# Kernel optimization log

Measured on AMD Instinct MI355X. Metric: run time of the kernel, lower is better.

## Reference

```python
import jax, jax.numpy as jnp
import numpy as np
import math

B, S, D = 8, 1024, 1024
NH, NKV, HD = 16, 8, 64
BLK_NUM, BLK_SIZE = 128, 8

def apply_rope(x, cos, sin):
    # x: (B,S,H,HD); cos/sin: (S, HD//2)
    x1 = x[..., 0::2]
    x2 = x[..., 1::2]
    c = cos[None, :, None, :]
    s = sin[None, :, None, :]
    r1 = x1 * c - x2 * s
    r2 = x1 * s + x2 * c
    out = jnp.stack([r1, r2], axis=-1).reshape(x.shape)
    return out

def setup_inputs() -> dict:
    key = jax.random.key(0)
    ks = jax.random.split(key, 7)
    x = jax.random.normal(ks[0], (B, S, D), dtype=jnp.float32)
    scale = 1.0 / math.sqrt(D)
    wq = jax.random.normal(ks[1], (D, NH * HD), dtype=jnp.float32) * scale
    wk = jax.random.normal(ks[2], (D, NKV * HD), dtype=jnp.float32) * scale
    wv = jax.random.normal(ks[3], (D, NKV * HD), dtype=jnp.float32) * scale
    wo = jax.random.normal(ks[4], (NH * HD, D), dtype=jnp.float32) * scale
    pos = jnp.arange(S, dtype=jnp.float32)
    inv_freq = 1.0 / (10000.0 ** (jnp.arange(0, HD, 2, dtype=jnp.float32) / HD))
    ang = pos[:, None] * inv_freq[None, :]
    freqs_cis_cos = jnp.cos(ang)
    freqs_cis_sin = jnp.sin(ang)
    return {"x": x, "wq": wq, "wk": wk, "wv": wv, "wo": wo,
            "freqs_cis_cos": freqs_cis_cos, "freqs_cis_sin": freqs_cis_sin,
            "start_pos": 0}

def reference(x, wq, wk, wv, wo, freqs_cis_cos, freqs_cis_sin, start_pos):
    q = (x @ wq).reshape(B, S, NH, HD)
    k = (x @ wk).reshape(B, S, NKV, HD)
    v = (x @ wv).reshape(B, S, NKV, HD)
    q = apply_rope(q, freqs_cis_cos, freqs_cis_sin)
    k = apply_rope(k, freqs_cis_cos, freqs_cis_sin)
    # GQA: repeat kv heads
    rep = NH // NKV
    k = jnp.repeat(k, rep, axis=2)  # (B,S,NH,HD)
    v = jnp.repeat(v, rep, axis=2)
    # block-causal mask: q in block i attends to kv blocks j <= i
    blk_id = jnp.arange(S) // BLK_SIZE
    mask = blk_id[:, None] >= blk_id[None, :]  # (S,S)
    scores = jnp.einsum('bqhd,bkhd->bhqk', q, k) / math.sqrt(HD)
    scores = jnp.where(mask[None, None], scores, -jnp.inf)
    attn = jax.nn.softmax(scores, axis=-1)
    out = jnp.einsum('bhqk,bkhd->bqhd', attn, v).reshape(B, S, NH * HD)
    return out @ wo
```

## Files before the change

kernel.cpp:

```cpp
#include <hip/hip_runtime.h>
#include <cstdint>
#include <math.h>

#define B_   8
#define S_   1024
#define D_   1024
#define NH_  16
#define NKV_ 8
#define HD_  64
#define M_   (B_*S_)

using bf16   = __bf16;
using bf16x4 = __attribute__((ext_vector_type(4))) __bf16;
using bf16x8 = __attribute__((ext_vector_type(8))) __bf16;
using f32x4  = __attribute__((ext_vector_type(4))) float;

__device__ __forceinline__ void gll16(const bf16* g, const bf16* l) {
    __builtin_amdgcn_global_load_lds(
        (const __attribute__((address_space(1))) unsigned int*)(uintptr_t)g,
        (__attribute__((address_space(3))) unsigned int*)(uintptr_t)l,
        16, 0, 0);
}

__device__ __forceinline__ void vm_wait0()  { asm volatile("s_waitcnt vmcnt(0)"  ::: "memory"); }
__device__ __forceinline__ void vm_wait5()  { asm volatile("s_waitcnt vmcnt(5)"  ::: "memory"); }
__device__ __forceinline__ void vm_wait6()  { asm volatile("s_waitcnt vmcnt(6)"  ::: "memory"); }
__device__ __forceinline__ void bar()       { __builtin_amdgcn_s_barrier(); asm volatile("" ::: "memory"); }

__global__ void k_prep1(const float* __restrict__ x,
                        const float* __restrict__ wq, const float* __restrict__ wk,
                        const float* __restrict__ wv, const float* __restrict__ wo,
                        bf16* __restrict__ xb, bf16* __restrict__ wqkvT, bf16* __restrict__ woT) {
    __shared__ float tile[64 * 65];
    int bid = blockIdx.x;
    int t = threadIdx.x;
    if (bid < 8192) {
        int i = bid * 256 + t;
        float4 v = ((const float4*)x)[i];
        bf16x4 o = { (bf16)v.x, (bf16)v.y, (bf16)v.z, (bf16)v.w };
        ((bf16x4*)xb)[i] = o;
        return;
    }
    int b2 = bid - 8192;
    int bx = b2 % 48, by = b2 / 48;
    const int R = 1024;
    const float* in; bf16* out; int C, xo;
    if (bx < 16)      { in = wq; out = wqkvT;               C = 1024; xo = bx; }
    else if (bx < 24) { in = wk; out = wqkvT + 1024 * 1024; C = 512;  xo = bx - 16; }
    else if (bx < 32) { in = wv; out = wqkvT + 1536 * 1024; C = 512;  xo = bx - 24; }
    else              { in = wo; out = woT;                 C = 1024; xo = bx - 32; }
    int r0 = by * 64, c0 = xo * 64;
    #pragma unroll
    for (int it = 0; it < 16; ++it) {
        int idx = it * 256 + t;
        int r = idx >> 6, c = idx & 63;
        tile[r * 65 + c] = in[(size_t)(r0 + r) * C + c0 + c];
    }
    __syncthreads();
    #pragma unroll
    for (int it = 0; it < 16; ++it) {
        int idx = it * 256 + t;
        int c = idx >> 6, r = idx & 63;
        out[(size_t)(c0 + c) * R + r0 + r] = (bf16)tile[r * 65 + c];
    }
}

template <typename OutT, int NI>
__global__ __launch_bounds__(512, 2) void k_gemm8p(const bf16* __restrict__ A,
                                                   const bf16* __restrict__ Bt,
                                                   OutT* __restrict__ C, int M, int N, int K) {
    constexpr int BN = NI * 64;
    __shared__ __align__(16) bf16 aL2[2 * 256 * 64];
    __shared__ __align__(16) bf16 bL2[2 * BN * 64];
    const int t    = threadIdx.x;
    const int lane = t & 63;
    const int w    = t >> 6;
    const int quad = lane >> 4;
    const int l16  = lane & 15;
    const int wr   = w >> 2;
    const int wc   = w & 3;

    int bid = blockIdx.y * gridDim.x + blockIdx.x;
    int cpx = (gridDim.x * gridDim.y) >> 3;
    int sw  = (bid & 7) * cpx + (bid >> 3);
    int bx  = sw % gridDim.x, by = sw / gridDim.x;
    const int m0 = by * 256;
    const int n0 = bx * BN;

    f32x4 acc[8][NI] = {};

    auto stageA2 = [&](int kb, int dbuf, int itX, int itY) {
        const int k0 = kb << 6;
        #pragma unroll
        for (int u = 0; u < 2; ++u) {
            int it = u ? itY : itX;
            int ci = it * 512 + t;
            int r = ci >> 3, c = ci & 7;
            int cg = c ^ (r & 7);
            gll16(A + (size_t)(m0 + r) * K + k0 + cg * 8, aL2 + dbuf * (256 * 64) + ci * 8);
        }
    };
    auto stageBh = [&](int kb, int dbuf, int nh) {
        const int k0 = kb << 6;
        #pragma unroll
        for (int j = 0; j < NI / 2; ++j) {
            int it = nh * (NI / 2) + j;
            int ci = it * 512 + t;
            int lr = ci >> 3, cs = ci & 7;
            int cg = cs ^ (lr & 7);
            int idx = lr - nh * (BN / 2);
            int wcc = idx / (NI * 8);
            int off = idx % (NI * 8);
            int g   = wcc * (NI * 16) + nh * (NI * 8) + off;
            gll16(Bt + (size_t)(n0 + g) * K + k0 + cg * 8, bL2 + dbuf * (BN * 64) + ci * 8);
        }
    };

    auto loadA = [&](const bf16* aL, int mh, bf16x8 (&af)[8]) {
        #pragma unroll
        for (int mi = 0; mi < 4; ++mi)
            #pragma unroll
            for (int kk = 0; kk < 2; ++kk) {
                int row = wr * 128 + (mh * 4 + mi) * 16 + l16;
                int ch  = (kk * 4 + quad) ^ (row & 7);
                af[mi * 2 + kk] = *(const bf16x8*)&aL[row * 64 + ch * 8];
            }
    };
    auto loadB = [&](const bf16* bL, int nh, bf16x8 (&bfr)[NI]) {
        #pragma unroll
        for (int j = 0; j < NI / 2; ++j)
            #pragma unroll
            for (int kk = 0; kk < 2; ++kk) {
                int lr = nh * (BN / 2) + wc * (NI * 8) + j * 16 + l16;
                int ch = (kk * 4 + quad) ^ (lr & 7);
                bfr[j * 2 + kk] = *(const bf16x8*)&bL[lr * 64 + ch * 8];
            }
    };
    auto mmac = [&](int mh, int nh, bf16x8 (&af)[8], bf16x8 (&bfr)[NI]) {
        __builtin_amdgcn_s_setprio(1);
        #pragma unroll
        for (int mi = 0; mi < 4; ++mi)
            #pragma unroll
            for (int j = 0; j < NI / 2; ++j)
                #pragma unroll
                for (int kk = 0; kk < 2; ++kk)
                    acc[mh * 4 + mi][nh * (NI / 2) + j] =
                        __builtin_amdgcn_mfma_f32_16x16x32_bf16(af[mi * 2 + kk], bfr[j * 2 + kk],
                                                                acc[mh * 4 + mi][nh * (NI / 2) + j], 0, 0, 0);
        __builtin_amdgcn_s_setprio(0);
    };

    const int NT = K >> 6;

    auto tile = [&](int T, int bufc) {
        const bf16* aL = aL2 + bufc * (256 * 64);
        const bf16* bL = bL2 + bufc * (BN * 64);
        bf16x8 af[8], bfr[NI];
        loadA(aL, 0, af); loadB(bL, 0, bfr);
        if (T + 1 < NT) stageBh(T + 1, bufc ^ 1, 1);
        bar();
        mmac(0, 0, af, bfr);
        bar();
        loadB(bL, 1, bfr);
        if (T + 2 < NT) stageA2(T + 2, bufc, 0, 2);
        bar();
        mmac(0, 1, af, bfr);
        bar();
        loadA(aL, 1, af); loadB(bL, 0, bfr);
        bar();
        mmac(1, 0, af, bfr);
        bar();
        loadB(bL, 1, bfr);
        if (T + 2 < NT) {
            stageA2(T + 2, bufc, 1, 3);
            stageBh(T + 2, bufc, 0);
            if constexpr (NI == 4) vm_wait6(); else vm_wait5();
        } else {
            vm_wait0();
        }
        bar();
        mmac(1, 1, af, bfr);
        bar();
    };

    stageA2(0, 0, 0, 2); stageA2(0, 0, 1, 3); stageBh(0, 0, 0); stageBh(0, 0, 1);
    stageA2(1, 1, 0, 2); stageA2(1, 1, 1, 3); stageBh(1, 1, 0);
    if constexpr (NI == 4) vm_wait6(); else vm_wait5();
    bar();

    for (int T = 0; T < NT; T += 2) {
        tile(T, 0);
        tile(T + 1, 1);
    }

    #pragma unroll
    for (int mi = 0; mi < 8; ++mi)
        #pragma unroll
        for (int ni = 0; ni < NI; ++ni)
            #pragma unroll
            for (int r = 0; r < 4; ++r) {
                int row = m0 + wr * 128 + mi * 16 + quad * 4 + r;
                int col = n0 + wc * (NI * 16) + ni * 16 + l16;
                C[(size_t)row * N + col] = (OutT)acc[mi][ni][r];
            }
}

__global__ void k_prep2(const bf16* __restrict__ qkv, const float* __restrict__ cosg,
                        const float* __restrict__ sing, bf16* __restrict__ qd,
                        bf16* __restrict__ kd, bf16* __restrict__ vt) {
    __shared__ __align__(16) bf16 tile[64 * 72];
    int bid = blockIdx.x;
    int t = threadIdx.x;
    if (bid < 8192) {
        if (t < 192) {
            int token = bid;
            int b = token >> 10, s = token & 1023;
            int hh = t >> 3, i8 = t & 7;
            float4 c4 = *(const float4*)&cosg[s * 32 + i8 * 4];
            float4 s4 = *(const float4*)&sing[s * 32 + i8 * 4];
            int srcBase, dstBase;
            bf16* dst;
            float sf;
            if (hh < 16) {
                srcBase = token * 2048 + hh * 64;
                dstBase = ((b * NH_ + hh) * S_ + s) * 64;
                dst = qd;
                sf = 0.180336879f;
            } else {
                int h = hh - 16;
                srcBase = token * 2048 + 1024 + h * 64;
                dstBase = ((b * NKV_ + h) * S_ + s) * 64;
                dst = kd;
                sf = 1.0f;
            }
            bf16x8 v = *(const bf16x8*)&qkv[srcBase + i8 * 8];
            const float cc[4] = { c4.x, c4.y, c4.z, c4.w };
            const float ss[4] = { s4.x, s4.y, s4.z, s4.w };
            bf16x8 o;
            #pragma unroll
            for (int j = 0; j < 4; ++j) {
                float e  = (float)v[2 * j];
                float od = (float)v[2 * j + 1];
                o[2 * j]     = (bf16)(sf * (e * cc[j] - od * ss[j]));
                o[2 * j + 1] = (bf16)(sf * (e * ss[j] + od * cc[j]));
            }
            *(bf16x8*)&dst[dstBase + i8 * 8] = o;
        }
        return;
    }
    int b2 = bid - 8192;
    int st = b2 & 15;
    int h  = (b2 >> 4) & 7;
    int b  = b2 >> 7;
    int s0 = st * 64;
    #pragma unroll
    for (int it = 0; it < 2; ++it) {
        int ci = it * 256 + t;
        int r = ci >> 3, c = ci & 7;
        *(uint4*)&tile[r * 72 + c * 8] =
            *(const uint4*)&qkv[(size_t)(b * S_ + s0 + r) * 2048 + 1536 + h * 64 + c * 8];
    }
    __syncthreads();
    #pragma unroll
    for (int it = 0; it < 2; ++it) {
        int ci = it * 256 + t;
        int d = ci >> 3, sc = ci & 7;
        int g = sc >> 2, q4 = sc & 3;
        bf16x8 v;
        #pragma unroll
        for (int j = 0; j < 8; ++j) {
            int s_ext = g * 32 + q4 * 4 + (j & 3) + 16 * (j >> 2);
            v[j] = tile[s_ext * 72 + d];
        }
        *(bf16x8*)&vt[(size_t)((b * NKV_ + h) * 64 + d) * S_ + s0 + sc * 8] = v;
    }
}

__global__ __launch_bounds__(256) void k_attn(const bf16* __restrict__ q, const bf16* __restrict__ k,
                                              const bf16* __restrict__ vt, bf16* __restrict__ out) {
    __shared__ __align__(16) bf16 kt[2 * 64 * 64];
    __shared__ __align__(16) bf16 vtt[2 * 64 * 64];
    int bid = blockIdx.x;
    int qt = 15 - (bid >> 7);
    int combo = bid & 127;
    int b = combo >> 4, h = combo & 15;
    int hkv = h >> 1;
    int t = threadIdx.x;
    int w = t >> 6, lane = t & 63, quad = lane >> 4, l16 = lane & 15;

    const bf16* qh = q + (size_t)(b * NH_ + h) * S_ * 64;
    int qw = qt * 64 + w * 16;
    const bf16* qb = qh + (size_t)(qw + l16) * 64;
    bf16x8 qf0 = *(const bf16x8*)(qb + quad * 8);
    bf16x8 qf1 = *(const bf16x8*)(qb + 32 + quad * 8);

    const bf16* kg = k  + (size_t)(b * NKV_ + hkv) * S_ * 64;
    const bf16* vg = vt + (size_t)(b * NKV_ + hkv) * 64 * S_;

    const int sr0 = t >> 3;
    const int cs  = t & 7;

    auto stage = [&](int u, int buf) {
        int k0 = u * 64;
        #pragma unroll
        for (int it = 0; it < 2; ++it) {
            int r  = sr0 + it * 32;
            int cg = cs ^ (r & 7);
            int ci = it * 256 + t;
            gll16(kg + (size_t)(k0 + r) * 64 + cg * 8, kt  + buf * 4096 + ci * 8);
            gll16(vg + (size_t)r * S_ + k0 + cg * 8,   vtt + buf * 4096 + ci * 8);
        }
    };

    const bf16 one = (bf16)1.0f;
    const bf16x8 vones = { one, one, one, one, one, one, one, one };

    f32x4 o[4] = {};
    f32x4 ol = {};
    const int klim = ((qw + l16) & ~7) + 8;

    auto unit = [&](int u, int buf, bool diag) {
        const bf16* ktb = kt  + buf * 4096;
        const bf16* vtb = vtt + buf * 4096;
        int k0 = u * 64;

        f32x4 sc[4] = {};
        #pragma unroll
        for (int kk = 0; kk < 2; ++kk)
            #pragma unroll
            for (int f = 0; f < 4; ++f) {
                int row = f * 16 + l16;
                int ch  = (kk * 4 + quad) ^ (row & 7);
                bf16x8 af = *(const bf16x8*)&ktb[row * 64 + ch * 8];
                sc[f] = __builtin_amdgcn_mfma_f32_16x16x32_bf16(af, kk ? qf1 : qf0, sc[f], 0, 0, 0);
            }

        float p[4][4];
        #pragma unroll
        for (int f = 0; f < 4; ++f)
            #pragma unroll
            for (int r = 0; r < 4; ++r) {
                float pv = __builtin_amdgcn_exp2f(sc[f][r]);
                if (diag && (k0 + f * 16 + quad * 4 + r >= klim)) pv = 0.f;
                p[f][r] = pv;
            }

        bf16x8 pa0, pa1;
        #pragma unroll
        for (int j = 0; j < 4; ++j) {
            pa0[j]     = (bf16)p[0][j];
            pa0[j + 4] = (bf16)p[1][j];
            pa1[j]     = (bf16)p[2][j];
            pa1[j + 4] = (bf16)p[3][j];
        }

        ol = __builtin_amdgcn_mfma_f32_16x16x32_bf16(pa0, vones, ol, 0, 0, 0);
        ol = __builtin_amdgcn_mfma_f32_16x16x32_bf16(pa1, vones, ol, 0, 0, 0);

        #pragma unroll
        for (int dc = 0; dc < 4; ++dc) {
            int row = dc * 16 + l16;
            #pragma unroll
            for (int kk = 0; kk < 2; ++kk) {
                int ch = (kk * 4 + quad) ^ (row & 7);
                bf16x8 vb = *(const bf16x8*)&vtb[row * 64 + ch * 8];
                o[dc] = __builtin_amdgcn_mfma_f32_16x16x32_bf16(kk ? pa1 : pa0, vb, o[dc], 0, 0, 0);
            }
        }
        vm_wait0();
        bar();
    };

    const int NU = qt + 1;
    stage(0, 0);
    vm_wait0();
    bar();

    int u = 0;
    for (; u + 2 <= NU; u += 2) {
        stage(u + 1, 1);
        unit(u, 0, false);
        if (u + 2 < NU) stage(u + 2, 0);
        unit(u + 1, 1, (u + 1) == NU - 1);
    }
    if (u < NU) unit(u, 0, true);

    #pragma unroll
    for (int r = 0; r < 4; ++r) {
        float invl = 1.0f / ol[r];
        #pragma unroll
        for (int dc = 0; dc < 4; ++dc) {
            int row = qw + quad * 4 + r;
            int col = h * 64 + dc * 16 + l16;
            out[(size_t)(b * S_ + row) * 1024 + col] = (bf16)(o[dc][r] * invl);
        }
    }
}

extern "C" void kernel_launch(void* const* d_in, const int* in_sizes, int n_in,
                              void* d_out, int out_size, void* d_ws, size_t ws_size,
                              hipStream_t stream) {
    const float* x  = (const float*)d_in[0];
    const float* wq = (const float*)d_in[1];
    const float* wk = (const float*)d_in[2];
    const float* wv = (const float*)d_in[3];
    const float* wo = (const float*)d_in[4];
    const float* fc = (const float*)d_in[5];
    const float* fs = (const float*)d_in[6];
    (void)in_sizes; (void)n_in; (void)out_size; (void)ws_size;

    char* ws = (char*)d_ws;
    bf16* xb    = (bf16*)(ws);
    bf16* wqkvT = (bf16*)(ws + (16u << 20));
    bf16* woT   = (bf16*)(ws + (20u << 20));
    bf16* qkvb  = (bf16*)(ws + (22u << 20));
    bf16* kb    = (bf16*)(ws + (54u << 20));
    bf16* vtb   = (bf16*)(ws + (62u << 20));
    bf16* qb    = xb;
    bf16* attnb = qkvb;

    k_prep1<<<dim3(8960), dim3(256), 0, stream>>>(x, wq, wk, wv, wo, xb, wqkvT, woT);

    k_gemm8p<bf16, 4><<<dim3(8, 32), dim3(512), 0, stream>>>(xb, wqkvT, qkvb, M_, 2048, 1024);

    k_prep2<<<dim3(9216), dim3(256), 0, stream>>>(qkvb, fc, fs, qb, kb, vtb);

    k_attn<<<dim3(2048), dim3(256), 0, stream>>>(qb, kb, vtb, attnb);

    k_gemm8p<float, 2><<<dim3(8, 32), dim3(512), 0, stream>>>(attnb, woT, (float*)d_out, M_, 1024, 1024);
}
```

Measured before the change: 202.8 us.

## Batch LDS reads with explicit waits and restructure attention double-buffer pipeline

```diff
diff --git a/kernel.cpp b/kernel.cpp
--- a/kernel.cpp
+++ b/kernel.cpp
@@ -22,7 +22,15 @@
         16, 0, 0);
 }
 
+__device__ __forceinline__ void dsr128(bf16x8& d, const bf16* p) {
+    asm volatile("ds_read_b128 %0, %1" : "=v"(d) : "v"((unsigned)(uintptr_t)p));
+}
+__device__ __forceinline__ void lgkm0() {
+    asm volatile("s_waitcnt lgkmcnt(0)" ::: "memory");
+    __builtin_amdgcn_sched_barrier(0);
+}
 __device__ __forceinline__ void vm_wait0()  { asm volatile("s_waitcnt vmcnt(0)"  ::: "memory"); }
+__device__ __forceinline__ void vm_wait4()  { asm volatile("s_waitcnt vmcnt(4)"  ::: "memory"); }
 __device__ __forceinline__ void vm_wait5()  { asm volatile("s_waitcnt vmcnt(5)"  ::: "memory"); }
 __device__ __forceinline__ void vm_wait6()  { asm volatile("s_waitcnt vmcnt(6)"  ::: "memory"); }
 __device__ __forceinline__ void bar()       { __builtin_amdgcn_s_barrier(); asm volatile("" ::: "memory"); }
@@ -123,7 +131,7 @@
             for (int kk = 0; kk < 2; ++kk) {
                 int row = wr * 128 + (mh * 4 + mi) * 16 + l16;
                 int ch  = (kk * 4 + quad) ^ (row & 7);
-                af[mi * 2 + kk] = *(const bf16x8*)&aL[row * 64 + ch * 8];
+                dsr128(af[mi * 2 + kk], &aL[row * 64 + ch * 8]);
             }
     };
     auto loadB = [&](const bf16* bL, int nh, bf16x8 (&bfr)[NI]) {
@@ -133,7 +141,7 @@
             for (int kk = 0; kk < 2; ++kk) {
                 int lr = nh * (BN / 2) + wc * (NI * 8) + j * 16 + l16;
                 int ch = (kk * 4 + quad) ^ (lr & 7);
-                bfr[j * 2 + kk] = *(const bf16x8*)&bL[lr * 64 + ch * 8];
+                dsr128(bfr[j * 2 + kk], &bL[lr * 64 + ch * 8]);
             }
     };
     auto mmac = [&](int mh, int nh, bf16x8 (&af)[8], bf16x8 (&bfr)[NI]) {
@@ -158,28 +166,24 @@
         bf16x8 af[8], bfr[NI];
         loadA(aL, 0, af); loadB(bL, 0, bfr);
         if (T + 1 < NT) stageBh(T + 1, bufc ^ 1, 1);
-        bar();
+        bar(); lgkm0();
         mmac(0, 0, af, bfr);
         bar();
         loadB(bL, 1, bfr);
         if (T + 2 < NT) stageA2(T + 2, bufc, 0, 2);
-        bar();
+        bar(); lgkm0();
         mmac(0, 1, af, bfr);
         bar();
         loadA(aL, 1, af); loadB(bL, 0, bfr);
-        bar();
+        bar(); lgkm0();
         mmac(1, 0, af, bfr);
         bar();
         loadB(bL, 1, bfr);
-        if (T + 2 < NT) {
-            stageA2(T + 2, bufc, 1, 3);
-            stageBh(T + 2, bufc, 0);
-            if constexpr (NI == 4) vm_wait6(); else vm_wait5();
-        } else {
-            vm_wait0();
-        }
-        bar();
+        if (T + 2 < NT) { stageA2(T + 2, bufc, 1, 3); stageBh(T + 2, bufc, 0); }
+        bar(); lgkm0();
         mmac(1, 1, af, bfr);
+        if (T + 2 < NT) { if constexpr (NI == 4) vm_wait6(); else vm_wait5(); }
+        else vm_wait0();
         bar();
     };
 
@@ -276,8 +280,8 @@
     }
 }
 
-__global__ __launch_bounds__(256) void k_attn(const bf16* __restrict__ q, const bf16* __restrict__ k,
-                                              const bf16* __restrict__ vt, bf16* __restrict__ out) {
+__global__ __launch_bounds__(256, 4) void k_attn(const bf16* __restrict__ q, const bf16* __restrict__ k,
+                                                 const bf16* __restrict__ vt, bf16* __restrict__ out) {
     __shared__ __align__(16) bf16 kt[2 * 64 * 64];
     __shared__ __align__(16) bf16 vtt[2 * 64 * 64];
     int bid = blockIdx.x;
@@ -319,20 +323,34 @@
     f32x4 ol = {};
     const int klim = ((qw + l16) & ~7) + 8;
 
-    auto unit = [&](int u, int buf, bool diag) {
-        const bf16* ktb = kt  + buf * 4096;
-        const bf16* vtb = vtt + buf * 4096;
-        int k0 = u * 64;
-
-        f32x4 sc[4] = {};
+    auto unit = [&](const bf16* ktb, const bf16* vtb, int k0, bool diag) {
+        bf16x8 af[8];
         #pragma unroll
         for (int kk = 0; kk < 2; ++kk)
             #pragma unroll
             for (int f = 0; f < 4; ++f) {
                 int row = f * 16 + l16;
                 int ch  = (kk * 4 + quad) ^ (row & 7);
-                bf16x8 af = *(const bf16x8*)&ktb[row * 64 + ch * 8];
-                sc[f] = __builtin_amdgcn_mfma_f32_16x16x32_bf16(af, kk ? qf1 : qf0, sc[f], 0, 0, 0);
+                dsr128(af[kk * 4 + f], &ktb[row * 64 + ch * 8]);
+            }
+        lgkm0();
+        f32x4 sc[4] = {};
+        __builtin_amdgcn_s_setprio(1);
+        #pragma unroll
+        for (int kk = 0; kk < 2; ++kk)
+            #pragma unroll
+            for (int f = 0; f < 4; ++f)
+                sc[f] = __builtin_amdgcn_mfma_f32_16x16x32_bf16(af[kk * 4 + f], kk ? qf1 : qf0, sc[f], 0, 0, 0);
+        __builtin_amdgcn_s_setprio(0);
+
+        bf16x8 vbf[8];
+        #pragma unroll
+        for (int dc = 0; dc < 4; ++dc)
+            #pragma unroll
+            for (int kk = 0; kk < 2; ++kk) {
+                int row = dc * 16 + l16;
+                int ch  = (kk * 4 + quad) ^ (row & 7);
+                dsr128(vbf[dc * 2 + kk], &vtb[row * 64 + ch * 8]);
             }
 
         float p[4][4];
@@ -344,7 +362,6 @@
                 if (diag && (k0 + f * 16 + quad * 4 + r >= klim)) pv = 0.f;
                 p[f][r] = pv;
             }
-
         bf16x8 pa0, pa1;
         #pragma unroll
         for (int j = 0; j < 4; ++j) {
@@ -353,37 +370,42 @@
             pa1[j]     = (bf16)p[2][j];
             pa1[j + 4] = (bf16)p[3][j];
         }
-
         ol = __builtin_amdgcn_mfma_f32_16x16x32_bf16(pa0, vones, ol, 0, 0, 0);
         ol = __builtin_amdgcn_mfma_f32_16x16x32_bf16(pa1, vones, ol, 0, 0, 0);
 
-        #pragma unroll
-        for (int dc = 0; dc < 4; ++dc) {
-            int row = dc * 16 + l16;
-            #pragma unroll
-            for (int kk = 0; kk < 2; ++kk) {
-                int ch = (kk * 4 + quad) ^ (row & 7);
-                bf16x8 vb = *(const bf16x8*)&vtb[row * 64 + ch * 8];
-                o[dc] = __builtin_amdgcn_mfma_f32_16x16x32_bf16(kk ? pa1 : pa0, vb, o[dc], 0, 0, 0);
-            }
-        }
-        vm_wait0();
-        bar();
+        lgkm0();
+        __builtin_amdgcn_s_setprio(1);
+        #pragma unroll
+        for (int dc = 0; dc < 4; ++dc)
+            #pragma unroll
+            for (int kk = 0; kk < 2; ++kk)
+                o[dc] = __builtin_amdgcn_mfma_f32_16x16x32_bf16(kk ? pa1 : pa0, vbf[dc * 2 + kk], o[dc], 0, 0, 0);
+        __builtin_amdgcn_s_setprio(0);
     };
 
     const int NU = qt + 1;
     stage(0, 0);
-    vm_wait0();
-    bar();
+    asm volatile("" :: "v"(qf0), "v"(qf1));
 
     int u = 0;
     for (; u + 2 <= NU; u += 2) {
+        bar();
         stage(u + 1, 1);
-        unit(u, 0, false);
-        if (u + 2 < NU) stage(u + 2, 0);
-        unit(u + 1, 1, (u + 1) == NU - 1);
-    }
-    if (u < NU) unit(u, 0, true);
+        vm_wait4();
+        bar();
+        unit(kt, vtt, u * 64, false);
+        bar();
+        bool hn = (u + 2 < NU);
+        if (hn) { stage(u + 2, 0); vm_wait4(); } else vm_wait0();
+        bar();
+        unit(kt + 4096, vtt + 4096, (u + 1) * 64, (u + 1) == NU - 1);
+    }
+    if (u < NU) {
+        bar();
+        vm_wait0();
+        bar();
+        unit(kt, vtt, u * 64, true);
+    }
 
     #pragma unroll
     for (int r = 0; r < 4; ++r) {
```

Measured after the change: 198.8 us. About the same (-2.0%).
